# Performance work log

Hardware: AMD Instinct MI355X
Metric: run time of the kernel (lower is better)

## Reference

```python
import jax, jax.numpy as jnp
import numpy as np

ATTN_SCALE = 0.12
HEAD_DIM = 128


def _rms_norm(x):
    # F.rms_norm with no weight; eps defaults to machine eps of dtype
    eps = jnp.asarray(jnp.finfo(x.dtype).eps, x.dtype)
    return x * jax.lax.rsqrt(jnp.mean(x * x, axis=-1, keepdims=True) + eps)


def _rope(x):
    # x: [B, T, H, D]; standard rotary over (first-half, second-half) pairs
    T, D = x.shape[1], x.shape[-1]
    half = D // 2
    inv_freq = 1.0 / (10000.0 ** (jnp.arange(half, dtype=jnp.float32) / half))
    ang = jnp.arange(T, dtype=jnp.float32)[:, None] * inv_freq[None, :]  # [T, half]
    cos = jnp.cos(ang)[None, :, None, :].astype(x.dtype)
    sin = jnp.sin(ang)[None, :, None, :].astype(x.dtype)
    x1, x2 = x[..., :half], x[..., half:]
    return jnp.concatenate([x1 * cos - x2 * sin, x1 * sin + x2 * cos], axis=-1)


def setup_inputs() -> dict:
    key = jax.random.key(0)
    ks = jax.random.split(key, 4)
    B, T, dim, H, hd = 4, 2048, 1024, 8, HEAD_DIM
    hdim = H * hd
    std = 0.5 * dim ** (-0.5)
    bound = (3.0 ** 0.5) * std
    return {
        "x": jax.random.normal(ks[0], (B, T, dim), jnp.float32),
        "ve": jax.random.normal(ks[1], (B, T, hdim), jnp.float32),
        "qkv_w": jax.random.uniform(ks[2], (3, hdim, dim), jnp.float32, -bound, bound),
        "lambdas": jnp.array([0.5, 0.5], jnp.float32),
        "c_proj_w": jax.random.normal(ks[3], (dim, hdim), jnp.float32) * (hdim ** -0.5),
        "c_proj_b": jnp.zeros((dim,), jnp.float32),
    }


def reference(x, ve, qkv_w, lambdas, c_proj_w, c_proj_b):
    B, T, dim = x.shape
    hdim = qkv_w.shape[1]
    hd = HEAD_DIM
    H = hdim // hd
    # fused QKV projection: [B,T,3,H,hd]
    qkv = jnp.einsum('btd,ehd->bteh', x, qkv_w.reshape(3 * hdim, dim).reshape(3 * H, hd, dim).reshape(3 * hdim // hd, hd, dim))
    qkv = jnp.einsum('btd,fd->btf', x, qkv_w.reshape(3 * hdim, dim)).reshape(B, T, 3, H, hd)
    q, k, v = qkv[:, :, 0], qkv[:, :, 1], qkv[:, :, 2]  # each [B,T,H,hd]
    q, k = _rms_norm(q), _rms_norm(k)
    q, k = _rope(q), _rope(k)
    v = lambdas[0] * v + lambdas[1] * ve.reshape(B, T, H, hd)
    # causal SDPA with custom scale
    scores = jnp.einsum('bthd,bshd->bhts', q, k) * ATTN_SCALE  # [B,H,T,T]
    causal = jnp.tril(jnp.ones((T, T), dtype=bool))
    scores = jnp.where(causal[None, None], scores, jnp.finfo(scores.dtype).min)
    p = jax.nn.softmax(scores, axis=-1)
    y = jnp.einsum('bhts,bshd->bthd', p, v).reshape(B, T, hdim)
    return y @ c_proj_w.T + c_proj_b
```

## Files before the change

kernel.cpp:

```cpp
#include <hip/hip_runtime.h>
#include <math.h>

typedef unsigned short u16;
typedef short bf16x8 __attribute__((ext_vector_type(8)));
typedef u16 u16x2 __attribute__((ext_vector_type(2)));
typedef u16 u16x4 __attribute__((ext_vector_type(4)));
typedef u16 u16x8 __attribute__((ext_vector_type(8)));
typedef float f32x2 __attribute__((ext_vector_type(2)));
typedef float f32x4 __attribute__((ext_vector_type(4)));
typedef float f32x16 __attribute__((ext_vector_type(16)));

typedef __attribute__((address_space(1))) const void gvoid_t;
typedef __attribute__((address_space(3))) void lvoid_t;

__device__ __forceinline__ u16 f2bf(float f) {
  union { float f; unsigned u; } v; v.f = f;
  unsigned r = v.u + 0x7fffu + ((v.u >> 16) & 1u);
  return (u16)(r >> 16);
}
__device__ __forceinline__ float bf2f(u16 h) {
  union { unsigned u; float f; } v; v.u = ((unsigned)h) << 16;
  return v.f;
}
__device__ __forceinline__ f32x4 mfma16(bf16x8 a, bf16x8 b, f32x4 c) {
  return __builtin_amdgcn_mfma_f32_16x16x32_bf16(a, b, c, 0, 0, 0);
}
__device__ __forceinline__ f32x16 mfma32(bf16x8 a, bf16x8 b, f32x16 c) {
  return __builtin_amdgcn_mfma_f32_32x32x16_bf16(a, b, c, 0, 0, 0);
}
__device__ __forceinline__ void gload_lds16(const void* g, void* l) {
  __builtin_amdgcn_global_load_lds((gvoid_t*)g, (lvoid_t*)l, 16, 0, 0);
}
__device__ __forceinline__ unsigned cvtpk_bf16(float lo, float hi) {
  unsigned r;
  asm("v_cvt_pk_bf16_f32 %0, %1, %2" : "=v"(r) : "v"(lo), "v"(hi));
  return r;
}
__device__ __forceinline__ void pswap32(unsigned& a, unsigned& b) {
  asm("v_permlane32_swap_b32 %0, %1" : "+v"(a), "+v"(b));
}

#define BAR() __builtin_amdgcn_s_barrier()
#define WAITLGKM()                          \
  asm volatile("s_waitcnt lgkmcnt(0)");     \
  __builtin_amdgcn_sched_barrier(0)
#define WAITVM2()                           \
  asm volatile("s_waitcnt vmcnt(2)");       \
  __builtin_amdgcn_sched_barrier(0)
#define WAITVM4()                           \
  asm volatile("s_waitcnt vmcnt(4)");       \
  __builtin_amdgcn_sched_barrier(0)

__global__ __launch_bounds__(256) void cvt_bf16_kernel(const float* __restrict__ in,
                                                       u16* __restrict__ out, int n4) {
  int i = blockIdx.x * 256 + threadIdx.x;
  if (i >= n4) return;
  f32x4 v = *(const f32x4*)(in + (size_t)i * 4);
  u16x4 o;
  o[0] = f2bf(v[0]); o[1] = f2bf(v[1]); o[2] = f2bf(v[2]); o[3] = f2bf(v[3]);
  *(u16x4*)(out + (size_t)i * 4) = o;
}

__global__ __launch_bounds__(256) void rope_tab_kernel(float* __restrict__ ct,
                                                       float* __restrict__ st) {
  int i = blockIdx.x * 256 + threadIdx.x;
  int t = i >> 6, j = i & 63;
  float inv = powf(10000.f, -(float)j * (1.0f / 64.0f));
  float ang = (float)t * inv;
  ct[i] = cosf(ang);
  st[i] = sinf(ang);
}

template <int OUTF32>
__global__ __launch_bounds__(512, 2) void gemm8p_kernel(
    const u16* __restrict__ A, const u16* __restrict__ B, void* __restrict__ C,
    const float* __restrict__ bias, int M, int N, int K, int nbn) {
  __shared__ u16 Alds[2][256 * 64];
  __shared__ u16 Blds[2][256 * 64];
  int nwg = gridDim.x;
  int cpx = nwg >> 3;
  int bid = blockIdx.x;
  int swz = (bid & 7) * cpx + (bid >> 3);
  int bm = swz / nbn, bn = swz % nbn;
  size_t m0 = (size_t)bm * 256, n0 = (size_t)bn * 256;
  int tid = threadIdx.x, wid = tid >> 6, lane = tid & 63;
  int wr = wid >> 2, wc = wid & 3, l15 = lane & 15, l4 = lane >> 4;
  int srow = tid >> 3, sch = tid & 7;

  const u16* Abase = A + m0 * K;
  const u16* Bbase = B + n0 * K;

  f32x4 acc[8][4];
#pragma unroll
  for (int m = 0; m < 8; m++)
#pragma unroll
    for (int n = 0; n < 4; n++) acc[m][n] = f32x4{0.f, 0.f, 0.f, 0.f};

  auto stageA = [&](int buf, int kt, int half) {
#pragma unroll
    for (int r = 0; r < 2; ++r) {
      int row = 128 * half + 64 * r + srow;
      gload_lds16(Abase + (size_t)row * K + kt * 64 + 8 * (sch ^ (row & 7)),
                  &Alds[buf][(128 * half + 64 * r + 8 * wid) * 64]);
    }
  };
  auto stageB = [&](int buf, int kt, int half) {
#pragma unroll
    for (int r = 0; r < 2; ++r) {
      int row = 128 * half + 64 * r + srow;
      gload_lds16(Bbase + (size_t)row * K + kt * 64 + 8 * (sch ^ (row & 7)),
                  &Blds[buf][(128 * half + 64 * r + 8 * wid) * 64]);
    }
  };
  auto rdA = [&](int buf, int half, bf16x8 (&a)[4][2]) {
#pragma unroll
    for (int mi = 0; mi < 4; ++mi)
#pragma unroll
      for (int kk = 0; kk < 2; ++kk) {
        int row = 128 * wr + 64 * half + 16 * mi + l15;
        a[mi][kk] = *(const bf16x8*)((const char*)(&Alds[buf][0]) + row * 128 +
                                     ((kk * 64 + 16 * l4) ^ ((row & 7) << 4)));
      }
  };
  auto rdB = [&](int buf, int half, bf16x8 (&bb)[2][2]) {
#pragma unroll
    for (int ni = 0; ni < 2; ++ni)
#pragma unroll
      for (int kk = 0; kk < 2; ++kk) {
        int row = 64 * wc + 32 * half + 16 * ni + l15;
        bb[ni][kk] = *(const bf16x8*)((const char*)(&Blds[buf][0]) + row * 128 +
                                      ((kk * 64 + 16 * l4) ^ ((row & 7) << 4)));
      }
  };

#define QUAD(AF, BF, MH, NH)                                              \
  do {                                                                    \
    __builtin_amdgcn_s_setprio(1);                                        \
    _Pragma("unroll") for (int mi = 0; mi < 4; ++mi)                      \
        _Pragma("unroll") for (int ni = 0; ni < 2; ++ni)                  \
            _Pragma("unroll") for (int kk = 0; kk < 2; ++kk)              \
                acc[4 * MH + mi][2 * NH + ni] =                           \
        mfma16(AF[mi][kk], BF[ni][kk], acc[4 * MH + mi][2 * NH + ni]);    \
    __builtin_amdgcn_s_setprio(0);                                        \
  } while (0)

  stageB(0, 0, 0);
  stageB(0, 0, 1);
  stageA(0, 0, 0);
  stageA(0, 0, 1);
  WAITVM2();
  BAR();

  int nk = K >> 6;
  bf16x8 a0[4][2], a1[4][2], b0[2][2], b1[2][2];
  for (int t = 0; t < nk; ++t) {
    int buf = t & 1, nxt = buf ^ 1;
    bool pf = (t + 1 < nk);
    rdA(buf, 0, a0);
    rdB(buf, 0, b0);
    if (pf) stageB(nxt, t + 1, 0);
    BAR();
    WAITLGKM();
    QUAD(a0, b0, 0, 0);
    BAR();
    rdB(buf, 1, b1);
    if (pf) stageB(nxt, t + 1, 1);
    BAR();
    WAITLGKM();
    QUAD(a0, b1, 0, 1);
    WAITVM4();
    BAR();
    rdA(buf, 1, a1);
    if (pf) stageA(nxt, t + 1, 0);
    BAR();
    WAITLGKM();
    QUAD(a1, b0, 1, 0);
    BAR();
    if (pf) stageA(nxt, t + 1, 1);
    BAR();
    QUAD(a1, b1, 1, 1);
    WAITVM2();
    BAR();
  }

#pragma unroll
  for (int mi = 0; mi < 8; ++mi) {
#pragma unroll
    for (int ni = 0; ni < 4; ++ni) {
      size_t row = m0 + 128 * wr + 16 * mi + 4 * l4;
      size_t col = n0 + 64 * wc + 16 * ni + l15;
#pragma unroll
      for (int i = 0; i < 4; ++i) {
        float v = acc[mi][ni][i];
        if constexpr (OUTF32) {
          ((float*)C)[(row + i) * N + col] = v + bias[col];
        } else {
          ((u16*)C)[(row + i) * N + col] = f2bf(v);
        }
      }
    }
  }
#undef QUAD
}

__global__ __launch_bounds__(256) void transform_kernel(
    const u16* __restrict__ qkv, const float* __restrict__ ve,
    const float* __restrict__ lam, const float* __restrict__ ct,
    const float* __restrict__ st, u16* __restrict__ qn, u16* __restrict__ kn,
    u16* __restrict__ vt) {
  constexpr int T = 2048, HD = 128;
  __shared__ u16 vtile[64][132];
  int tt = blockIdx.x, bh = blockIdx.y;
  int b = bh >> 3, h = bh & 7;
  int tid = threadIdx.x, wid = tid >> 6, lane = tid & 63;
  float l0 = lam[0], l1 = lam[1];
  int d0 = 2 * lane;
  float sgn = (lane < 32) ? -1.f : 1.f;
#pragma unroll 1
  for (int j = 0; j < 16; ++j) {
    int tl = wid * 16 + j;
    int t = tt * 64 + tl;
    size_t base = ((size_t)(b * T + t)) * 3072 + h * HD + d0;
    u16x2 qraw = *(const u16x2*)(qkv + base);
    u16x2 kraw = *(const u16x2*)(qkv + base + 1024);
    u16x2 vraw = *(const u16x2*)(qkv + base + 2048);
    f32x2 vef = *(const f32x2*)(ve + ((size_t)(b * T + t)) * 1024 + h * HD + d0);
    float q0 = bf2f(qraw[0]), q1 = bf2f(qraw[1]);
    float k0 = bf2f(kraw[0]), k1 = bf2f(kraw[1]);
    float sq = q0 * q0 + q1 * q1, sk = k0 * k0 + k1 * k1;
#pragma unroll
    for (int m = 1; m < 64; m <<= 1) {
      sq += __shfl_xor(sq, m);
      sk += __shfl_xor(sk, m);
    }
    float qs = rsqrtf(sq * (1.f / 128.f) + 1.1920929e-7f);
    float ks = rsqrtf(sk * (1.f / 128.f) + 1.1920929e-7f);
    q0 *= qs; q1 *= qs; k0 *= ks; k1 *= ks;
    int jj = d0 & 63;
    f32x2 c2 = *(const f32x2*)(ct + t * 64 + jj);
    f32x2 s2 = *(const f32x2*)(st + t * 64 + jj);
    float q0p = __shfl_xor(q0, 32), q1p = __shfl_xor(q1, 32);
    float k0p = __shfl_xor(k0, 32), k1p = __shfl_xor(k1, 32);
    u16x2 oq, ok;
    oq[0] = f2bf(q0 * c2[0] + sgn * q0p * s2[0]);
    oq[1] = f2bf(q1 * c2[1] + sgn * q1p * s2[1]);
    ok[0] = f2bf(k0 * c2[0] + sgn * k0p * s2[0]);
    ok[1] = f2bf(k1 * c2[1] + sgn * k1p * s2[1]);
    size_t orow = ((size_t)bh * T + t) * HD + d0;
    *(u16x2*)(qn + orow) = oq;
    *(u16x2*)(kn + orow) = ok;
    vtile[tl][d0] = f2bf(l0 * bf2f(vraw[0]) + l1 * vef[0]);
    vtile[tl][d0 + 1] = f2bf(l0 * bf2f(vraw[1]) + l1 * vef[1]);
  }
  __syncthreads();
#pragma unroll
  for (int it = 0; it < 4; ++it) {
    int ci = it * 256 + tid;
    int d = ci >> 3, c8 = ci & 7;
    u16x8 o;
#pragma unroll
    for (int u = 0; u < 8; u++) o[u] = vtile[c8 * 8 + u][d];
    *(u16x8*)(vt + ((size_t)bh * HD + d) * T + tt * 64 + c8 * 8) = o;
  }
}

__global__ __launch_bounds__(256, 2) void attn_kernel(
    const u16* __restrict__ Qn, const u16* __restrict__ Kn,
    const u16* __restrict__ Vt, u16* __restrict__ Y) {
  constexpr int T = 2048;
  __shared__ u16 Klds[2][64 * 128];
  __shared__ u16 Vlds[2][128 * 64];
  int bid = blockIdx.x;
  int s = 15 - (bid >> 5);
  int bh = bid & 31;
  int b = bh >> 3, h = bh & 7;
  int tid = threadIdx.x, wid = tid >> 6, lane = tid & 63;
  int l31 = lane & 31, hh = lane >> 5;
  const u16* Qb = Qn + (size_t)bh * T * 128;
  const u16* Kb = Kn + (size_t)bh * T * 128;
  const u16* Vb = Vt + (size_t)bh * 128 * T;
  int q0w = s * 128 + wid * 32;
  int qmaxw = q0w + 31;
  int ktend = 2 * s + 2;
  int qg = q0w + l31;

  bf16x8 qf[8];
  {
    const u16* qr = Qb + (size_t)(q0w + l31) * 128 + 8 * hh;
#pragma unroll
    for (int ks = 0; ks < 8; ks++) qf[ks] = *(const bf16x8*)(qr + 16 * ks);
  }
  f32x16 acc[4];
#pragma unroll
  for (int mt = 0; mt < 4; mt++)
#pragma unroll
    for (int r = 0; r < 16; r++) acc[mt][r] = 0.f;
  float m_run = -1e30f, l_run = 0.f;

  auto stage = [&](int buf, int kt) {
#pragma unroll
    for (int it = 0; it < 4; ++it) {
      int id = wid * 256 + it * 64 + lane;
      int r = id >> 4, c = id & 15;
      gload_lds16(Kb + (size_t)(kt * 64 + r) * 128 + 8 * (c ^ (r & 7)),
                  &Klds[buf][(size_t)(wid * 256 + it * 64) * 8]);
      int rv = id >> 3, cv = id & 7;
      gload_lds16(Vb + (size_t)rv * T + kt * 64 + 8 * (cv ^ (rv & 7)),
                  &Vlds[buf][(size_t)(wid * 256 + it * 64) * 8]);
    }
  };

  stage(0, 0);
  __syncthreads();

  for (int kt = 0; kt < ktend; ++kt) {
    int cur = kt & 1;
    if (kt + 1 < ktend) stage(cur ^ 1, kt + 1);
    if (kt * 64 <= qmaxw) {
      const char* kb = (const char*)&Klds[cur][0];
      const char* vb = (const char*)&Vlds[cur][0];
      int rswz = (l31 & 7) << 4;
      f32x16 st0, st1;
#pragma unroll
      for (int r = 0; r < 16; r++) { st0[r] = 0.f; st1[r] = 0.f; }
#pragma unroll
      for (int ks = 0; ks < 8; ks++) {
        bf16x8 kf0 = *(const bf16x8*)(kb + ((l31 * 256 + 32 * ks + 16 * hh) ^ rswz));
        bf16x8 kf1 = *(const bf16x8*)(kb + (((32 + l31) * 256 + 32 * ks + 16 * hh) ^ rswz));
        st0 = mfma32(kf0, qf[ks], st0);
        st1 = mfma32(kf1, qf[ks], st1);
      }
      bool edge = (kt == (qmaxw >> 6));
      if (edge) {
#pragma unroll
        for (int r = 0; r < 16; r++) {
          int kvb = kt * 64 + (r & 3) + 8 * (r >> 2) + 4 * hh;
          st0[r] = (kvb > qg) ? -1e30f : st0[r] * 0.12f;
          st1[r] = (kvb + 32 > qg) ? -1e30f : st1[r] * 0.12f;
        }
      } else {
#pragma unroll
        for (int r = 0; r < 16; r++) { st0[r] *= 0.12f; st1[r] *= 0.12f; }
      }
      float m8[8];
#pragma unroll
      for (int r = 0; r < 8; r++)
        m8[r] = fmaxf(fmaxf(st0[r], st0[r + 8]), fmaxf(st1[r], st1[r + 8]));
#pragma unroll
      for (int r = 0; r < 4; r++) m8[r] = fmaxf(m8[r], m8[r + 4]);
      float pm = fmaxf(fmaxf(m8[0], m8[1]), fmaxf(m8[2], m8[3]));
      pm = fmaxf(pm, __shfl_xor(pm, 32));
      float mnew = fmaxf(m_run, pm);
      float alpha = __expf(m_run - mnew);
      m_run = mnew;
      float sa = 0.f, sb = 0.f, sc = 0.f, sd = 0.f;
#pragma unroll
      for (int r = 0; r < 4; r++) {
        st0[r]      = __expf(st0[r]      - mnew); sa += st0[r];
        st0[r + 4]  = __expf(st0[r + 4]  - mnew); sb += st0[r + 4];
        st0[r + 8]  = __expf(st0[r + 8]  - mnew); sc += st0[r + 8];
        st0[r + 12] = __expf(st0[r + 12] - mnew); sd += st0[r + 12];
        st1[r]      = __expf(st1[r]      - mnew); sa += st1[r];
        st1[r + 4]  = __expf(st1[r + 4]  - mnew); sb += st1[r + 4];
        st1[r + 8]  = __expf(st1[r + 8]  - mnew); sc += st1[r + 8];
        st1[r + 12] = __expf(st1[r + 12] - mnew); sd += st1[r + 12];
      }
      float ps = (sa + sb) + (sc + sd);
      ps += __shfl_xor(ps, 32);
      l_run = l_run * alpha + ps;
#pragma unroll
      for (int mt = 0; mt < 4; mt++)
#pragma unroll
        for (int r = 0; r < 16; r++) acc[mt][r] *= alpha;
      unsigned pA0[4], pB0[4], pA1[4], pB1[4];
#pragma unroll
      for (int rr = 0; rr < 4; rr++) {
        pA0[rr] = cvtpk_bf16(st0[4 * rr], st0[4 * rr + 1]);
        pB0[rr] = cvtpk_bf16(st0[4 * rr + 2], st0[4 * rr + 3]);
        pA1[rr] = cvtpk_bf16(st1[4 * rr], st1[4 * rr + 1]);
        pB1[rr] = cvtpk_bf16(st1[4 * rr + 2], st1[4 * rr + 3]);
      }
      bf16x8 pf[4];
#pragma unroll
      for (int ks2 = 0; ks2 < 4; ks2++) {
        int k1 = ks2 & 1;
        unsigned a0, b0, a1, b1;
        if (ks2 < 2) { a0 = pA0[2 * k1]; b0 = pA0[2 * k1 + 1]; a1 = pB0[2 * k1]; b1 = pB0[2 * k1 + 1]; }
        else         { a0 = pA1[2 * k1]; b0 = pA1[2 * k1 + 1]; a1 = pB1[2 * k1]; b1 = pB1[2 * k1 + 1]; }
        pswap32(a0, b0);
        pswap32(a1, b1);
        union { unsigned w[4]; bf16x8 v; } u;
        u.w[0] = a0; u.w[1] = a1; u.w[2] = b0; u.w[3] = b1;
        pf[ks2] = u.v;
      }
#pragma unroll
      for (int mt = 0; mt < 4; mt++) {
        int row = 32 * mt + l31;
#pragma unroll
        for (int ks2 = 0; ks2 < 4; ks2++) {
          bf16x8 vf = *(const bf16x8*)(vb + ((row * 128 + 32 * ks2 + 16 * hh) ^ rswz));
          acc[mt] = mfma32(vf, pf[ks2], acc[mt]);
        }
      }
    }
    __syncthreads();
  }
  float linv = 1.f / l_run;
  size_t yrow = (size_t)b * T + q0w + l31;
  u16* yp = Y + yrow * 1024 + h * 128;
#pragma unroll
  for (int mt = 0; mt < 4; mt++) {
#pragma unroll
    for (int rr = 0; rr < 4; rr++) {
      u16x4 o;
#pragma unroll
      for (int i = 0; i < 4; i++) o[i] = f2bf(acc[mt][4 * rr + i] * linv);
      *(u16x4*)(yp + 32 * mt + 8 * rr + 4 * hh) = o;
    }
  }
}

extern "C" void kernel_launch(void* const* d_in, const int* in_sizes, int n_in,
                              void* d_out, int out_size, void* d_ws, size_t ws_size,
                              hipStream_t stream) {
  (void)in_sizes; (void)n_in; (void)out_size; (void)ws_size;
  const float* x = (const float*)d_in[0];
  const float* ve = (const float*)d_in[1];
  const float* qkvw = (const float*)d_in[2];
  const float* lam = (const float*)d_in[3];
  const float* cpw = (const float*)d_in[4];
  const float* cpb = (const float*)d_in[5];
  float* out = (float*)d_out;
  char* ws = (char*)d_ws;

  u16* xb   = (u16*)(ws + 0);
  u16* wqkv = (u16*)(ws + 16777216);
  u16* wp   = (u16*)(ws + 23068672);
  u16* qkv  = (u16*)(ws + 25165824);
  u16* qn   = (u16*)(ws + 75497472);
  u16* kn   = (u16*)(ws + 92274688);
  u16* vt   = (u16*)(ws + 109051904);
  float* ctab = (float*)(ws + 125829120);
  float* stab = (float*)(ws + 126353408);
  u16* y = xb;

  rope_tab_kernel<<<512, 256, 0, stream>>>(ctab, stab);
  cvt_bf16_kernel<<<8192, 256, 0, stream>>>(x, xb, 2097152);
  cvt_bf16_kernel<<<3072, 256, 0, stream>>>(qkvw, wqkv, 786432);
  cvt_bf16_kernel<<<1024, 256, 0, stream>>>(cpw, wp, 262144);
  gemm8p_kernel<0><<<384, 512, 0, stream>>>(xb, wqkv, qkv, nullptr, 8192, 3072, 1024, 12);
  transform_kernel<<<dim3(32, 32), 256, 0, stream>>>(qkv, ve, lam, ctab, stab, qn, kn, vt);
  attn_kernel<<<512, 256, 0, stream>>>(qn, kn, vt, y);
  gemm8p_kernel<1><<<128, 512, 0, stream>>>(y, wp, out, cpb, 8192, 1024, 1024, 4);
}
```

Baseline: 209.8 us.

## Use 128-row GEMM tiles, lazy softmax rescale, and reorder attention blocks

Templates the GEMM on an M tile size and launches both projections with 128-row tiles, which doubles the grid so more blocks are available to fill the compute units. Launch bounds move from two blocks to one block per SIMD. The attention kernel now folds the scale into the exp via an FMA and skips the running-max rescale of the accumulators unless the max grows by more than a threshold. It also interleaves heavy and light causal query blocks in the block order to balance the work. This trades less reuse per GEMM tile and a looser max bound on the exponentials for lower VALU cost and better load balance.

```diff
diff --git a/kernel.cpp b/kernel.cpp
--- a/kernel.cpp
+++ b/kernel.cpp
@@ -44,11 +44,8 @@
 #define WAITLGKM()                          \
   asm volatile("s_waitcnt lgkmcnt(0)");     \
   __builtin_amdgcn_sched_barrier(0)
-#define WAITVM2()                           \
-  asm volatile("s_waitcnt vmcnt(2)");       \
-  __builtin_amdgcn_sched_barrier(0)
-#define WAITVM4()                           \
-  asm volatile("s_waitcnt vmcnt(4)");       \
+#define WAITVM(N)                                \
+  asm volatile("s_waitcnt vmcnt(" #N ")");       \
   __builtin_amdgcn_sched_barrier(0)
 
 __global__ __launch_bounds__(256) void cvt_bf16_kernel(const float* __restrict__ in,
@@ -71,18 +68,23 @@
   st[i] = sinf(ang);
 }
 
-template <int OUTF32>
-__global__ __launch_bounds__(512, 2) void gemm8p_kernel(
+template <int BM, int OUTF32>
+__global__ __launch_bounds__(512, 1) void gemm8p_kernel(
     const u16* __restrict__ A, const u16* __restrict__ B, void* __restrict__ C,
     const float* __restrict__ bias, int M, int N, int K, int nbn) {
-  __shared__ u16 Alds[2][256 * 64];
+  constexpr int AH = BM / 2;
+  constexpr int WR = AH / 2;
+  constexpr int MI = WR / 16;
+  constexpr int NACC = 2 * MI;
+  constexpr int AROUNDS = AH / 64;
+  __shared__ u16 Alds[2][BM * 64];
   __shared__ u16 Blds[2][256 * 64];
   int nwg = gridDim.x;
   int cpx = nwg >> 3;
   int bid = blockIdx.x;
   int swz = (bid & 7) * cpx + (bid >> 3);
   int bm = swz / nbn, bn = swz % nbn;
-  size_t m0 = (size_t)bm * 256, n0 = (size_t)bn * 256;
+  size_t m0 = (size_t)bm * BM, n0 = (size_t)bn * 256;
   int tid = threadIdx.x, wid = tid >> 6, lane = tid & 63;
   int wr = wid >> 2, wc = wid & 3, l15 = lane & 15, l4 = lane >> 4;
   int srow = tid >> 3, sch = tid & 7;
@@ -90,18 +92,18 @@
   const u16* Abase = A + m0 * K;
   const u16* Bbase = B + n0 * K;
 
-  f32x4 acc[8][4];
-#pragma unroll
-  for (int m = 0; m < 8; m++)
+  f32x4 acc[NACC][4];
+#pragma unroll
+  for (int m = 0; m < NACC; m++)
 #pragma unroll
     for (int n = 0; n < 4; n++) acc[m][n] = f32x4{0.f, 0.f, 0.f, 0.f};
 
   auto stageA = [&](int buf, int kt, int half) {
 #pragma unroll
-    for (int r = 0; r < 2; ++r) {
-      int row = 128 * half + 64 * r + srow;
+    for (int r = 0; r < AROUNDS; ++r) {
+      int row = AH * half + 64 * r + srow;
       gload_lds16(Abase + (size_t)row * K + kt * 64 + 8 * (sch ^ (row & 7)),
-                  &Alds[buf][(128 * half + 64 * r + 8 * wid) * 64]);
+                  &Alds[buf][(AH * half + 64 * r + 8 * wid) * 64]);
     }
   };
   auto stageB = [&](int buf, int kt, int half) {
@@ -112,12 +114,12 @@
                   &Blds[buf][(128 * half + 64 * r + 8 * wid) * 64]);
     }
   };
-  auto rdA = [&](int buf, int half, bf16x8 (&a)[4][2]) {
-#pragma unroll
-    for (int mi = 0; mi < 4; ++mi)
+  auto rdA = [&](int buf, int half, bf16x8 (&a)[MI][2]) {
+#pragma unroll
+    for (int mi = 0; mi < MI; ++mi)
 #pragma unroll
       for (int kk = 0; kk < 2; ++kk) {
-        int row = 128 * wr + 64 * half + 16 * mi + l15;
+        int row = AH * half + WR * wr + 16 * mi + l15;
         a[mi][kk] = *(const bf16x8*)((const char*)(&Alds[buf][0]) + row * 128 +
                                      ((kk * 64 + 16 * l4) ^ ((row & 7) << 4)));
       }
@@ -136,11 +138,11 @@
 #define QUAD(AF, BF, MH, NH)                                              \
   do {                                                                    \
     __builtin_amdgcn_s_setprio(1);                                        \
-    _Pragma("unroll") for (int mi = 0; mi < 4; ++mi)                      \
+    _Pragma("unroll") for (int mi = 0; mi < MI; ++mi)                     \
         _Pragma("unroll") for (int ni = 0; ni < 2; ++ni)                  \
             _Pragma("unroll") for (int kk = 0; kk < 2; ++kk)              \
-                acc[4 * MH + mi][2 * NH + ni] =                           \
-        mfma16(AF[mi][kk], BF[ni][kk], acc[4 * MH + mi][2 * NH + ni]);    \
+                acc[MI * MH + mi][2 * NH + ni] =                          \
+        mfma16(AF[mi][kk], BF[ni][kk], acc[MI * MH + mi][2 * NH + ni]);   \
     __builtin_amdgcn_s_setprio(0);                                        \
   } while (0)
 
@@ -148,11 +150,11 @@
   stageB(0, 0, 1);
   stageA(0, 0, 0);
   stageA(0, 0, 1);
-  WAITVM2();
+  if constexpr (BM == 256) { WAITVM(2); } else { WAITVM(1); }
   BAR();
 
   int nk = K >> 6;
-  bf16x8 a0[4][2], a1[4][2], b0[2][2], b1[2][2];
+  bf16x8 a0[MI][2], a1[MI][2], b0[2][2], b1[2][2];
   for (int t = 0; t < nk; ++t) {
     int buf = t & 1, nxt = buf ^ 1;
     bool pf = (t + 1 < nk);
@@ -168,7 +170,7 @@
     BAR();
     WAITLGKM();
     QUAD(a0, b1, 0, 1);
-    WAITVM4();
+    if (pf) { WAITVM(4); } else { WAITVM(0); }
     BAR();
     rdA(buf, 1, a1);
     if (pf) stageA(nxt, t + 1, 0);
@@ -179,15 +181,17 @@
     if (pf) stageA(nxt, t + 1, 1);
     BAR();
     QUAD(a1, b1, 1, 1);
-    WAITVM2();
-    BAR();
-  }
-
-#pragma unroll
-  for (int mi = 0; mi < 8; ++mi) {
+    if (pf) {
+      if constexpr (BM == 256) { WAITVM(2); } else { WAITVM(1); }
+    }
+    BAR();
+  }
+
+#pragma unroll
+  for (int mi = 0; mi < NACC; ++mi) {
 #pragma unroll
     for (int ni = 0; ni < 4; ++ni) {
-      size_t row = m0 + 128 * wr + 16 * mi + 4 * l4;
+      size_t row = m0 + AH * (mi / MI) + WR * wr + 16 * (mi % MI) + 4 * l4;
       size_t col = n0 + 64 * wc + 16 * ni + l15;
 #pragma unroll
       for (int i = 0; i < 4; ++i) {
@@ -271,7 +275,8 @@
   __shared__ u16 Klds[2][64 * 128];
   __shared__ u16 Vlds[2][128 * 64];
   int bid = blockIdx.x;
-  int s = 15 - (bid >> 5);
+  int g = bid >> 5;
+  int s = (g < 8) ? (15 - g) : (g - 8);
   int bh = bid & 31;
   int b = bh >> 3, h = bh & 7;
   int tid = threadIdx.x, wid = tid >> 6, lane = tid & 63;
@@ -335,12 +340,9 @@
 #pragma unroll
         for (int r = 0; r < 16; r++) {
           int kvb = kt * 64 + (r & 3) + 8 * (r >> 2) + 4 * hh;
-          st0[r] = (kvb > qg) ? -1e30f : st0[r] * 0.12f;
-          st1[r] = (kvb + 32 > qg) ? -1e30f : st1[r] * 0.12f;
+          if (kvb > qg) st0[r] = -1e30f;
+          if (kvb + 32 > qg) st1[r] = -1e30f;
         }
-      } else {
-#pragma unroll
-        for (int r = 0; r < 16; r++) { st0[r] *= 0.12f; st1[r] *= 0.12f; }
       }
       float m8[8];
 #pragma unroll
@@ -350,28 +352,33 @@
       for (int r = 0; r < 4; r++) m8[r] = fmaxf(m8[r], m8[r + 4]);
       float pm = fmaxf(fmaxf(m8[0], m8[1]), fmaxf(m8[2], m8[3]));
       pm = fmaxf(pm, __shfl_xor(pm, 32));
-      float mnew = fmaxf(m_run, pm);
-      float alpha = __expf(m_run - mnew);
-      m_run = mnew;
+      float pmn = pm * 0.12f;
+      bool nos = __all(pmn <= m_run + 8.0f);
+      float mnew = nos ? m_run : fmaxf(m_run, pmn);
+      if (!nos) {
+        float alpha = __expf(m_run - mnew);
+        l_run *= alpha;
+#pragma unroll
+        for (int mt = 0; mt < 4; mt++)
+#pragma unroll
+          for (int r = 0; r < 16; r++) acc[mt][r] *= alpha;
+        m_run = mnew;
+      }
       float sa = 0.f, sb = 0.f, sc = 0.f, sd = 0.f;
 #pragma unroll
       for (int r = 0; r < 4; r++) {
-        st0[r]      = __expf(st0[r]      - mnew); sa += st0[r];
-        st0[r + 4]  = __expf(st0[r + 4]  - mnew); sb += st0[r + 4];
-        st0[r + 8]  = __expf(st0[r + 8]  - mnew); sc += st0[r + 8];
-        st0[r + 12] = __expf(st0[r + 12] - mnew); sd += st0[r + 12];
-        st1[r]      = __expf(st1[r]      - mnew); sa += st1[r];
-        st1[r + 4]  = __expf(st1[r + 4]  - mnew); sb += st1[r + 4];
-        st1[r + 8]  = __expf(st1[r + 8]  - mnew); sc += st1[r + 8];
-        st1[r + 12] = __expf(st1[r + 12] - mnew); sd += st1[r + 12];
+        st0[r]      = __expf(fmaf(st0[r],      0.12f, -mnew)); sa += st0[r];
+        st0[r + 4]  = __expf(fmaf(st0[r + 4],  0.12f, -mnew)); sb += st0[r + 4];
+        st0[r + 8]  = __expf(fmaf(st0[r + 8],  0.12f, -mnew)); sc += st0[r + 8];
+        st0[r + 12] = __expf(fmaf(st0[r + 12], 0.12f, -mnew)); sd += st0[r + 12];
+        st1[r]      = __expf(fmaf(st1[r],      0.12f, -mnew)); sa += st1[r];
+        st1[r + 4]  = __expf(fmaf(st1[r + 4],  0.12f, -mnew)); sb += st1[r + 4];
+        st1[r + 8]  = __expf(fmaf(st1[r + 8],  0.12f, -mnew)); sc += st1[r + 8];
+        st1[r + 12] = __expf(fmaf(st1[r + 12], 0.12f, -mnew)); sd += st1[r + 12];
       }
       float ps = (sa + sb) + (sc + sd);
       ps += __shfl_xor(ps, 32);
-      l_run = l_run * alpha + ps;
-#pragma unroll
-      for (int mt = 0; mt < 4; mt++)
-#pragma unroll
-        for (int r = 0; r < 16; r++) acc[mt][r] *= alpha;
+      l_run += ps;
       unsigned pA0[4], pB0[4], pA1[4], pB1[4];
 #pragma unroll
       for (int rr = 0; rr < 4; rr++) {
@@ -448,8 +455,8 @@
   cvt_bf16_kernel<<<8192, 256, 0, stream>>>(x, xb, 2097152);
   cvt_bf16_kernel<<<3072, 256, 0, stream>>>(qkvw, wqkv, 786432);
   cvt_bf16_kernel<<<1024, 256, 0, stream>>>(cpw, wp, 262144);
-  gemm8p_kernel<0><<<384, 512, 0, stream>>>(xb, wqkv, qkv, nullptr, 8192, 3072, 1024, 12);
+  gemm8p_kernel<128, 0><<<768, 512, 0, stream>>>(xb, wqkv, qkv, nullptr, 8192, 3072, 1024, 12);
   transform_kernel<<<dim3(32, 32), 256, 0, stream>>>(qkv, ve, lam, ctab, stab, qn, kn, vt);
   attn_kernel<<<512, 256, 0, stream>>>(qn, kn, vt, y);
-  gemm8p_kernel<1><<<128, 512, 0, stream>>>(y, wp, out, cpb, 8192, 1024, 1024, 4);
-}
+  gemm8p_kernel<128, 1><<<256, 512, 0, stream>>>(y, wp, out, cpb, 8192, 1024, 1024, 4);
+}
```

After: 209.8 us. Within noise of the previous version (+0.0%).
